# Optimization experiments

Hardware: AMD Instinct MI355X
Metric: run time of the kernel (lower is better)

## Reference

```python
import jax, jax.numpy as jnp
import numpy as np

N, G, D, H, B = 32768, 1024, 512, 768, 4   # nodes, graphs, hidden, shared, branches
GHD, NHD = 64, 3                           # graph head dim, node head dim (var_output=1)

def setup_inputs() -> dict:
    key = jax.random.key(0)
    ks = jax.random.split(key, 8)
    scale = 0.02
    x = jax.random.normal(ks[0], (N, D), dtype=jnp.float32)
    batch = jnp.sort(jax.random.randint(ks[1], (N,), 0, G, dtype=jnp.int32))
    dataset_name = jax.random.randint(ks[2], (G,), 0, B, dtype=jnp.int32)
    return {
        "x": x,
        "batch": batch,
        "dataset_name": dataset_name,
        "Wg_shared": jax.random.normal(ks[3], (B, D, H), jnp.float32) * scale,
        "bg_shared": jnp.zeros((B, H), jnp.float32),
        "Wg_head": jax.random.normal(ks[4], (B, H, 2 * GHD), jnp.float32) * scale,
        "bg_head": jnp.zeros((B, 2 * GHD), jnp.float32),
        "Wn1": jax.random.normal(ks[5], (B, D, D), jnp.float32) * scale,
        "bn1": jnp.zeros((B, D), jnp.float32),
        "Wn2": jax.random.normal(ks[6], (B, D, 2 * NHD), jnp.float32) * scale,
        "bn2": jnp.zeros((B, 2 * NHD), jnp.float32),
    }

def _select_branch(y, branch_ids):
    # y: [n, B, f], branch_ids: [n] -> [n, f]
    return jnp.take_along_axis(y, branch_ids[:, None, None], axis=1)[:, 0]

def reference(x, batch, dataset_name, Wg_shared, bg_shared, Wg_head, bg_head,
              Wn1, bn1, Wn2, bn2):
    nG = dataset_name.shape[0]
    # --- graph mean pooling (graph_pool_fn with reduction='mean') ---
    counts = jax.ops.segment_sum(jnp.ones((x.shape[0], 1), x.dtype), batch,
                                 num_segments=nG)
    x_graph = jax.ops.segment_sum(x, batch, num_segments=nG) / jnp.maximum(counts, 1.0)
    # --- graph head: per-dataset-ID branch dispatch (dense-MoE form) ---
    hg = jax.nn.relu(jnp.einsum('gd,bdh->gbh', x_graph, Wg_shared) + bg_shared)  # [G,B,H]
    hg_sel = _select_branch(hg, dataset_name)                                    # [G,H]
    og = jnp.einsum('gh,bho->gbo', hg_sel, Wg_head) + bg_head                    # [G,B,2*GHD]
    og_sel = _select_branch(og, dataset_name)
    graph_head = og_sel[:, :GHD]
    graph_var = og_sel[:, GHD:] ** 2
    # --- node head: route nodes by their graph's dataset ID (repeat_interleave) ---
    node_branch = dataset_name[batch]                                            # [N]
    hn = jax.nn.relu(jnp.einsum('nd,bdh->nbh', x, Wn1) + bn1)                    # [N,B,D]
    hn_sel = _select_branch(hn, node_branch)                                     # [N,D]
    on = jnp.einsum('nh,bho->nbo', hn_sel, Wn2) + bn2                            # [N,B,2*NHD]
    on_sel = _select_branch(on, node_branch)
    node_head = on_sel[:, :NHD]
    node_var = on_sel[:, NHD:] ** 2
    # torch returns (outputs, outputs_var); flattened here as 4 arrays
    return (graph_head, node_head, graph_var, node_var)
```

## Files before the change

kernel.cpp:

```cpp
#include <hip/hip_runtime.h>

#define N_NODES 32768
#define G_GRAPHS 1024
#define D_DIM 512
#define H_DIM 768
#define B_BR 4
#define GHD 64
#define NHD 3

#define NH_OFF (G_GRAPHS * GHD)
#define GV_OFF (G_GRAPHS * GHD + N_NODES * NHD)
#define NV_OFF (2 * G_GRAPHS * GHD + N_NODES * NHD)

typedef unsigned short ushort_t;
typedef __attribute__((ext_vector_type(8))) short short8;
typedef __attribute__((ext_vector_type(4))) float f32x4;
typedef __attribute__((ext_vector_type(4))) ushort_t ushort4_t;

__device__ __forceinline__ ushort_t rne_bf16(float v) {
  unsigned bits = __float_as_uint(v);
  return (ushort_t)((bits + 0x7fffu + ((bits >> 16) & 1u)) >> 16);
}

__global__ __launch_bounds__(1024) void segscan_kernel(
    const int* __restrict__ batch, const int* __restrict__ dsname,
    int* __restrict__ gstart, int* __restrict__ goff, int* __restrict__ glist,
    int* __restrict__ cnt, int* __restrict__ gcnt, int* __restrict__ pbase) {
  __shared__ int sg[G_GRAPHS + 1];
  __shared__ int scnt[4], sgcnt[4];
  const int tid = threadIdx.x;
  {
    int g = tid;
    int lo = 0, hi = N_NODES;
    while (lo < hi) { int mid = (lo + hi) >> 1; if (batch[mid] < g) lo = mid + 1; else hi = mid; }
    sg[g] = lo; gstart[g] = lo;
    if (tid == 0) { sg[G_GRAPHS] = N_NODES; gstart[G_GRAPHS] = N_NODES; }
  }
  __syncthreads();
  if (tid < 256) {
    const int lane = tid & 63;
    const int b = tid >> 6;
    int run_n = 0, run_g = 0;
    for (int c = 0; c < G_GRAPHS / 64; ++c) {
      int g = c * 64 + lane;
      int mine = (dsname[g] == b) ? 1 : 0;
      int len = mine ? (sg[g + 1] - sg[g]) : 0;
      int sl = len, so = mine;
#pragma unroll
      for (int off = 1; off < 64; off <<= 1) {
        int tl = __shfl_up(sl, off);
        int to = __shfl_up(so, off);
        if (lane >= off) { sl += tl; so += to; }
      }
      if (mine) {
        goff[g] = run_n + sl - len;
        glist[b * G_GRAPHS + run_g + so - 1] = g;
      }
      run_n += __shfl(sl, 63);
      run_g += __shfl(so, 63);
    }
    if (lane == 0) { scnt[b] = run_n; sgcnt[b] = run_g; }
  }
  __syncthreads();
  if (tid == 0) {
    int p = 0;
    for (int b2 = 0; b2 < 4; ++b2) {
      cnt[b2] = scnt[b2];
      gcnt[b2] = sgcnt[b2];
      pbase[b2] = p;
      p += (scnt[b2] + 63) & ~63;
    }
  }
}

__global__ __launch_bounds__(256) void prep_kernel(
    const float* __restrict__ x, const int* __restrict__ batch,
    const int* __restrict__ dsname, const int* __restrict__ gstart,
    const int* __restrict__ goff, const int* __restrict__ pbase,
    int* __restrict__ lists, ushort_t* __restrict__ xp,
    ushort_t* __restrict__ xgb,
    const float* __restrict__ Wn1, ushort_t* __restrict__ WPh,
    const float* __restrict__ Wg1, ushort_t* __restrict__ WG1,
    const float* __restrict__ Wgh, ushort_t* __restrict__ WG2,
    const float* __restrict__ Wn2, ushort_t* __restrict__ W2T) {
  __shared__ float Ws[64][65];
  const int bid = blockIdx.x;
  const int tid = threadIdx.x;

  if (bid < 1024) {
    const int rl = tid >> 6;
    const int cs = tid & 63;
    const int g = bid;
    const int start = gstart[g];
    const int len = gstart[g + 1] - start;
    const int b = dsname[g];
    const int og = goff[g];
    const int off0 = pbase[b] + og;
    float s0 = 0.f, s1 = 0.f, s2 = 0.f, s3 = 0.f;
    float s4 = 0.f, s5 = 0.f, s6 = 0.f, s7 = 0.f;
    for (int i = rl; i < len; i += 4) {
      int n = start + i;
      const float* sp = x + (size_t)n * D_DIM + cs * 8;
      float4 v0 = *reinterpret_cast<const float4*>(sp);
      float4 v1 = *reinterpret_cast<const float4*>(sp + 4);
      s0 += v0.x; s1 += v0.y; s2 += v0.z; s3 += v0.w;
      s4 += v1.x; s5 += v1.y; s6 += v1.z; s7 += v1.w;
      short8 h;
      h[0] = (short)rne_bf16(v0.x); h[1] = (short)rne_bf16(v0.y);
      h[2] = (short)rne_bf16(v0.z); h[3] = (short)rne_bf16(v0.w);
      h[4] = (short)rne_bf16(v1.x); h[5] = (short)rne_bf16(v1.y);
      h[6] = (short)rne_bf16(v1.z); h[7] = (short)rne_bf16(v1.w);
      int ib = og + i;
      *reinterpret_cast<short8*>(xp + (size_t)(off0 + i) * 512 + (cs ^ (ib & 7)) * 8) = h;
      if (cs == 0) lists[b * N_NODES + ib] = n;
    }
    float* red = (float*)Ws;
    float* rr = red + (rl * 64 + cs) * 8;
    rr[0] = s0; rr[1] = s1; rr[2] = s2; rr[3] = s3;
    rr[4] = s4; rr[5] = s5; rr[6] = s6; rr[7] = s7;
    __syncthreads();
    if (rl == 0) {
      float inv = (len > 0) ? 1.0f / (float)len : 0.0f;
      short8 h;
#pragma unroll
      for (int k = 0; k < 8; ++k) {
        float tot = red[(0 * 64 + cs) * 8 + k] + red[(1 * 64 + cs) * 8 + k] +
                    red[(2 * 64 + cs) * 8 + k] + red[(3 * 64 + cs) * 8 + k];
        h[k] = (short)rne_bf16(tot * inv);
      }
      *reinterpret_cast<short8*>(xgb + (size_t)g * D_DIM + cs * 8) = h;
    }
  } else {
    const int cid = bid - 1024;
    if (cid < 256) {
      int b = cid >> 6, t = cid & 63;
      int kt = t >> 3, nt = t & 7;
      const float* W = Wn1 + (size_t)b * D_DIM * D_DIM;
      for (int i = tid; i < 64 * 64; i += 256) {
        int k = i >> 6, n = i & 63;
        Ws[k][n] = W[(size_t)(kt * 64 + k) * D_DIM + nt * 64 + n];
      }
      __syncthreads();
      for (int i = tid; i < 64 * 8; i += 256) {
        int n = i >> 3, kq8 = i & 7;
        short8 sh;
#pragma unroll
        for (int j = 0; j < 8; ++j) sh[j] = (short)rne_bf16(Ws[kq8 * 8 + j][n]);
        int gn = nt * 64 + n, gk0 = kt * 64 + kq8 * 8;
        int n16 = gn >> 4, l15 = gn & 15;
        int ks = gk0 >> 5, lq = (gk0 >> 3) & 3;
        size_t off = ((((size_t)b * 32 + n16) * 16 + ks) * 64 + lq * 16 + l15) * 8;
        *reinterpret_cast<short8*>(WPh + off) = sh;
      }
    } else if (cid < 640) {
      int l2 = cid - 256;
      int b = l2 / 96, t = l2 % 96;
      int kt = t / 12, nt = t % 12;
      const float* W = Wg1 + (size_t)b * D_DIM * H_DIM;
      for (int i = tid; i < 64 * 64; i += 256) {
        int k = i >> 6, n = i & 63;
        Ws[k][n] = W[(size_t)(kt * 64 + k) * H_DIM + nt * 64 + n];
      }
      __syncthreads();
      for (int i = tid; i < 64 * 8; i += 256) {
        int n = i >> 3, kq8 = i & 7;
        short8 sh;
#pragma unroll
        for (int j = 0; j < 8; ++j) sh[j] = (short)rne_bf16(Ws[kq8 * 8 + j][n]);
        int gn = nt * 64 + n, gk0 = kt * 64 + kq8 * 8;
        int n16 = gn >> 4, l15 = gn & 15;
        int ks = gk0 >> 5, lq = (gk0 >> 3) & 3;
        size_t off = ((((size_t)b * 48 + n16) * 16 + ks) * 64 + lq * 16 + l15) * 8;
        *reinterpret_cast<short8*>(WG1 + off) = sh;
      }
    } else if (cid < 644) {
      int b = cid - 640;
      const float* W = Wgh + (size_t)b * H_DIM * 2 * GHD;
      for (int i = tid; i < 8 * 24 * 64; i += 256) {
        int n16 = i / (24 * 64);
        int rem = i % (24 * 64);
        int ks = rem / 64, lane = rem % 64;
        int l15 = lane & 15, lq = lane >> 4;
        int o = n16 * 16 + l15;
        short8 sv;
#pragma unroll
        for (int j = 0; j < 8; ++j) {
          int k = ks * 32 + lq * 8 + j;
          sv[j] = (short)rne_bf16(W[(size_t)k * 128 + o]);
        }
        *reinterpret_cast<short8*>(WG2 + (size_t)i * 8 + (size_t)b * (8 * 24 * 64 * 8)) = sv;
      }
    } else {
      int b = cid - 644;
      for (int i = tid; i < 16 * D_DIM; i += 256) {
        int o = i & 15, c = i >> 4;
        float v = (o < 6) ? Wn2[(size_t)b * D_DIM * 6 + c * 6 + o] : 0.0f;
        W2T[(size_t)b * 16 * D_DIM + o * D_DIM + c] = rne_bf16(v);
      }
    }
  }
}

#define NBM 64
#define GRAPH_BLOCKS 128
#define NODE_BLOCKS 576

__global__ __launch_bounds__(512, 2) void mega_kernel(
    const ushort_t* __restrict__ xpacked,
    const ushort_t* __restrict__ WPh,
    const float* __restrict__ bn1,
    const ushort_t* __restrict__ W2T, const float* __restrict__ bn2,
    const int* __restrict__ cnt, const int* __restrict__ pbase,
    const int* __restrict__ lists,
    const ushort_t* __restrict__ xgb,
    const ushort_t* __restrict__ WG1, const float* __restrict__ bg_shared,
    const ushort_t* __restrict__ WG2, const float* __restrict__ bg_head,
    const int* __restrict__ gcnt, const int* __restrict__ glist,
    float* __restrict__ out) {
  __shared__ __align__(16) char smem[131072];
  __shared__ int idxbuf[64];

  const int bid = blockIdx.x;
  const int tid = threadIdx.x;
  const int lane = tid & 63;
  const int w = tid >> 6;
  const int l15 = lane & 15;
  const int lq = lane >> 4;

  if (bid >= GRAPH_BLOCKS) {
    const int nb = bid - GRAPH_BLOCKS;
    const int b = (nb & 7) >> 1;
    const int tile = ((nb >> 3) << 1) | (nb & 1);
    const int count = cnt[b];
    const int base = tile * NBM;
    if (base >= count) return;
    const int tile_base = pbase[b] + base;

    ushort_t* Ah = (ushort_t*)smem;
    if (tid < NBM) {
      int r = base + tid;
      idxbuf[tid] = (r < count) ? lists[b * N_NODES + r] : lists[b * N_NODES];
    }

    const char* srow = (const char*)(xpacked + (size_t)tile_base * 512);
#pragma unroll
    for (int i = 0; i < 8; ++i) {
      int row = w * 8 + i;
      const void* gsrc = srow + (size_t)row * 1024 + (size_t)lane * 16;
      __builtin_amdgcn_global_load_lds(
          (const __attribute__((address_space(1))) void*)gsrc,
          (__attribute__((address_space(3))) void*)((char*)Ah + row * 1024),
          16, 0, 0);
    }
    __syncthreads();

    const ushort_t* __restrict__ wph =
        WPh + (((size_t)b * 32 + w * 4) * 16) * 512 + (size_t)lane * 8;
    ushort_t* Bl = (ushort_t*)(smem + 65536 + w * 8192);

#pragma unroll
    for (int ct = 0; ct < 4; ++ct) {
      __builtin_amdgcn_global_load_lds(
          (const __attribute__((address_space(1))) void*)(wph + (size_t)(ct * 16) * 512),
          (__attribute__((address_space(3))) void*)(Bl + ct * 512),
          16, 0, 0);
    }

    f32x4 acc[4][4];
#pragma unroll
    for (int i = 0; i < 4; ++i)
#pragma unroll
      for (int j = 0; j < 4; ++j) acc[i][j] = (f32x4){0.f, 0.f, 0.f, 0.f};

#pragma unroll
    for (int ks = 0; ks < 16; ++ks) {
      const int nks = (ks + 1) & 15;
      ushort_t* Bnx = Bl + ((ks + 1) & 1) * 2048;
#pragma unroll
      for (int ct = 0; ct < 4; ++ct) {
        __builtin_amdgcn_global_load_lds(
            (const __attribute__((address_space(1))) void*)(wph + (size_t)(ct * 16 + nks) * 512),
            (__attribute__((address_space(3))) void*)(Bnx + ct * 512),
            16, 0, 0);
      }
      asm volatile("s_waitcnt vmcnt(4)" ::: "memory");
      __builtin_amdgcn_sched_barrier(0);
      const ushort_t* Bc = Bl + (ks & 1) * 2048;
      short8 ah[4], bh[4];
#pragma unroll
      for (int rt = 0; rt < 4; ++rt) {
        int R = rt * 16 + l15;
        int byteoff = R * 1024 + ((ks * 64 + lq * 16) ^ ((R & 7) << 4));
        ah[rt] = *reinterpret_cast<const short8*>((const char*)Ah + byteoff);
      }
#pragma unroll
      for (int ct = 0; ct < 4; ++ct)
        bh[ct] = *reinterpret_cast<const short8*>(Bc + ct * 512 + lane * 8);
#pragma unroll
      for (int ct = 0; ct < 4; ++ct) {
#pragma unroll
        for (int rt = 0; rt < 4; ++rt) {
          acc[rt][ct] = __builtin_amdgcn_mfma_f32_16x16x32_bf16(ah[rt], bh[ct], acc[rt][ct], 0, 0, 0);
        }
      }
    }

    __syncthreads();
    ushort_t* hn = Ah;
#pragma unroll
    for (int ct = 0; ct < 4; ++ct) {
      int n = w * 64 + ct * 16 + l15;
      float bias = bn1[b * D_DIM + n];
#pragma unroll
      for (int rt = 0; rt < 4; ++rt) {
#pragma unroll
        for (int j = 0; j < 4; ++j) {
          int row = rt * 16 + lq * 4 + j;
          float v = fmaxf(acc[rt][ct][j] + bias, 0.0f);
          int byteoff = row * 1024 + ((n * 2) ^ ((row & 7) << 4));
          *reinterpret_cast<ushort_t*>((char*)hn + byteoff) = rne_bf16(v);
        }
      }
    }
    __syncthreads();

    if (w < 4) {
      f32x4 acc2 = (f32x4){0.f, 0.f, 0.f, 0.f};
      const ushort_t* __restrict__ w2 =
          W2T + (size_t)b * (16 * 512) + (size_t)l15 * 512 + lq * 8;
      const int R = w * 16 + l15;
#pragma unroll
      for (int ks = 0; ks < 16; ++ks) {
        int byteoff = R * 1024 + ((ks * 64 + lq * 16) ^ ((R & 7) << 4));
        short8 a2 = *reinterpret_cast<const short8*>((const char*)hn + byteoff);
        short8 b2 = *reinterpret_cast<const short8*>(w2 + ks * 32);
        acc2 = __builtin_amdgcn_mfma_f32_16x16x32_bf16(a2, b2, acc2, 0, 0, 0);
      }
      int o = l15;
      if (o < 6) {
        float bo = bn2[b * 6 + o];
#pragma unroll
        for (int j = 0; j < 4; ++j) {
          int r = w * 16 + lq * 4 + j;
          if (base + r < count) {
            int n = idxbuf[r];
            float v = acc2[j] + bo;
            if (o < NHD) out[NH_OFF + n * NHD + o] = v;
            else out[NV_OFF + n * NHD + (o - NHD)] = v * v;
          }
        }
      }
    }
  } else {
    const int gb = bid;
    const int b = (gb & 7) >> 1;
    const int tile = ((gb >> 3) << 1) | (gb & 1);
    const int gc = gcnt[b];
    const int base = tile * 32;
    if (base >= gc) return;

    ushort_t* Ag = (ushort_t*)smem;
    if (tid < 32) {
      int r = base + tid;
      idxbuf[tid] = (r < gc) ? glist[b * G_GRAPHS + r] : glist[b * G_GRAPHS];
    }
    __syncthreads();

#pragma unroll
    for (int it = 0; it < 4; ++it) {
      int u = it * 512 + tid;
      int r = u >> 6, cp = u & 63;
      const ushort_t* sp = xgb + (size_t)idxbuf[r] * D_DIM + cp * 8;
      short8 h = *reinterpret_cast<const short8*>(sp);
      int byteoff = r * 1024 + ((cp * 16) ^ ((r & 7) << 4));
      *reinterpret_cast<short8*>((char*)Ag + byteoff) = h;
    }
    __syncthreads();

    f32x4 acc[2][6];
#pragma unroll
    for (int i = 0; i < 2; ++i)
#pragma unroll
      for (int j = 0; j < 6; ++j) acc[i][j] = (f32x4){0.f, 0.f, 0.f, 0.f};

    const ushort_t* __restrict__ g1 =
        WG1 + (((size_t)b * 48 + w * 6) * 16) * 512 + (size_t)lane * 8;

    for (int ks = 0; ks < 16; ++ks) {
      short8 ah[2];
#pragma unroll
      for (int rt = 0; rt < 2; ++rt) {
        int R = rt * 16 + l15;
        int byteoff = R * 1024 + ((ks * 64 + lq * 16) ^ ((R & 7) << 4));
        ah[rt] = *reinterpret_cast<const short8*>((const char*)Ag + byteoff);
      }
#pragma unroll
      for (int ct = 0; ct < 6; ++ct) {
        short8 bh = *reinterpret_cast<const short8*>(g1 + (size_t)(ct * 16 + ks) * 512);
#pragma unroll
        for (int rt = 0; rt < 2; ++rt) {
          acc[rt][ct] = __builtin_amdgcn_mfma_f32_16x16x32_bf16(ah[rt], bh, acc[rt][ct], 0, 0, 0);
        }
      }
    }

    __syncthreads();
    ushort_t* hgs = (ushort_t*)smem;
#pragma unroll
    for (int ct = 0; ct < 6; ++ct) {
      int n = w * 96 + ct * 16 + l15;
      float bias = bg_shared[b * H_DIM + n];
#pragma unroll
      for (int rt = 0; rt < 2; ++rt) {
#pragma unroll
        for (int j = 0; j < 4; ++j) {
          int row = rt * 16 + lq * 4 + j;
          float v = fmaxf(acc[rt][ct][j] + bias, 0.0f);
          int byteoff = row * 1536 + ((n * 2) ^ ((row & 7) << 4));
          *reinterpret_cast<ushort_t*>((char*)hgs + byteoff) = rne_bf16(v);
        }
      }
    }
    __syncthreads();

    f32x4 acc2[2];
    acc2[0] = (f32x4){0.f, 0.f, 0.f, 0.f};
    acc2[1] = (f32x4){0.f, 0.f, 0.f, 0.f};
    const ushort_t* __restrict__ g2 =
        WG2 + ((size_t)(b * 8 + w) * 24 * 64 + lane) * 8;

    for (int ks = 0; ks < 24; ++ks) {
      short8 b2 = *reinterpret_cast<const short8*>(g2 + (size_t)ks * 512);
#pragma unroll
      for (int rt = 0; rt < 2; ++rt) {
        int R = rt * 16 + l15;
        int byteoff = R * 1536 + ((ks * 64 + lq * 16) ^ ((R & 7) << 4));
        short8 a2 = *reinterpret_cast<const short8*>((const char*)hgs + byteoff);
        acc2[rt] = __builtin_amdgcn_mfma_f32_16x16x32_bf16(a2, b2, acc2[rt], 0, 0, 0);
      }
    }

    int o = w * 16 + l15;
    float bo = bg_head[b * 2 * GHD + o];
#pragma unroll
    for (int rt = 0; rt < 2; ++rt) {
#pragma unroll
      for (int j = 0; j < 4; ++j) {
        int r = rt * 16 + lq * 4 + j;
        if (base + r < gc) {
          int g = idxbuf[r];
          float v = acc2[rt][j] + bo;
          if (o < GHD) out[g * GHD + o] = v;
          else out[GV_OFF + g * GHD + (o - GHD)] = v * v;
        }
      }
    }
  }
}

extern "C" void kernel_launch(void* const* d_in, const int* in_sizes, int n_in,
                              void* d_out, int out_size, void* d_ws, size_t ws_size,
                              hipStream_t stream) {
  const float* x         = (const float*)d_in[0];
  const int*   batch     = (const int*)d_in[1];
  const int*   dsname    = (const int*)d_in[2];
  const float* Wg_shared = (const float*)d_in[3];
  const float* bg_shared = (const float*)d_in[4];
  const float* Wg_head   = (const float*)d_in[5];
  const float* bg_head   = (const float*)d_in[6];
  const float* Wn1       = (const float*)d_in[7];
  const float* bn1       = (const float*)d_in[8];
  const float* Wn2       = (const float*)d_in[9];
  const float* bn2       = (const float*)d_in[10];
  float* out = (float*)d_out;

  int* ws_i   = (int*)d_ws;
  int* cnt    = ws_i;
  int* gcnt   = ws_i + 8;
  int* pbase  = ws_i + 12;
  int* gstart = ws_i + 16;
  int* goff   = ws_i + 1056;
  int* glist  = ws_i + 2080;
  int* lists  = ws_i + 6176;
  ushort_t* xgb  = (ushort_t*)(ws_i + 137248);
  ushort_t* WPh  = xgb + 524288;
  ushort_t* W2T  = WPh + 1048576;
  ushort_t* WG1  = W2T + 32768;
  ushort_t* WG2  = WG1 + 1572864;
  ushort_t* xpacked = WG2 + 393216;

  segscan_kernel<<<1, 1024, 0, stream>>>(batch, dsname, gstart, goff, glist,
                                         cnt, gcnt, pbase);
  prep_kernel<<<1672, 256, 0, stream>>>(x, batch, dsname, gstart, goff, pbase,
                                        lists, xpacked, xgb,
                                        Wn1, WPh, Wg_shared, WG1,
                                        Wg_head, WG2, Wn2, W2T);
  mega_kernel<<<GRAPH_BLOCKS + NODE_BLOCKS, 512, 0, stream>>>(
      xpacked, WPh, bn1, W2T, bn2, cnt, pbase, lists,
      xgb, WG1, bg_shared, WG2, bg_head, gcnt, glist, out);
}
```

Baseline: 91.98 us.

## Gather and convert x to bf16 inside node GEMM instead of prepacking

The prep kernel no longer writes a branch-packed bf16 copy of x. Instead, each node tile in the main kernel gathers its rows from fp32 x through the index list, converts them to bf16, and stores them into swizzled LDS. This removes a 32 MB bf16 write and its later read, at the cost of uncoalesced-by-row fp32 gathers (twice the bytes per row) and synchronous loads rather than async global-to-LDS copies inside the GEMM kernel.

```diff
diff --git a/kernel.cpp b/kernel.cpp
--- a/kernel.cpp
+++ b/kernel.cpp
@@ -76,8 +76,8 @@
 __global__ __launch_bounds__(256) void prep_kernel(
     const float* __restrict__ x, const int* __restrict__ batch,
     const int* __restrict__ dsname, const int* __restrict__ gstart,
-    const int* __restrict__ goff, const int* __restrict__ pbase,
-    int* __restrict__ lists, ushort_t* __restrict__ xp,
+    const int* __restrict__ goff,
+    int* __restrict__ lists,
     ushort_t* __restrict__ xgb,
     const float* __restrict__ Wn1, ushort_t* __restrict__ WPh,
     const float* __restrict__ Wg1, ushort_t* __restrict__ WG1,
@@ -95,24 +95,15 @@
     const int len = gstart[g + 1] - start;
     const int b = dsname[g];
     const int og = goff[g];
-    const int off0 = pbase[b] + og;
+    for (int i = tid; i < len; i += 256) lists[b * N_NODES + og + i] = start + i;
     float s0 = 0.f, s1 = 0.f, s2 = 0.f, s3 = 0.f;
     float s4 = 0.f, s5 = 0.f, s6 = 0.f, s7 = 0.f;
     for (int i = rl; i < len; i += 4) {
-      int n = start + i;
-      const float* sp = x + (size_t)n * D_DIM + cs * 8;
+      const float* sp = x + (size_t)(start + i) * D_DIM + cs * 8;
       float4 v0 = *reinterpret_cast<const float4*>(sp);
       float4 v1 = *reinterpret_cast<const float4*>(sp + 4);
       s0 += v0.x; s1 += v0.y; s2 += v0.z; s3 += v0.w;
       s4 += v1.x; s5 += v1.y; s6 += v1.z; s7 += v1.w;
-      short8 h;
-      h[0] = (short)rne_bf16(v0.x); h[1] = (short)rne_bf16(v0.y);
-      h[2] = (short)rne_bf16(v0.z); h[3] = (short)rne_bf16(v0.w);
-      h[4] = (short)rne_bf16(v1.x); h[5] = (short)rne_bf16(v1.y);
-      h[6] = (short)rne_bf16(v1.z); h[7] = (short)rne_bf16(v1.w);
-      int ib = og + i;
-      *reinterpret_cast<short8*>(xp + (size_t)(off0 + i) * 512 + (cs ^ (ib & 7)) * 8) = h;
-      if (cs == 0) lists[b * N_NODES + ib] = n;
     }
     float* red = (float*)Ws;
     float* rr = red + (rl * 64 + cs) * 8;
@@ -206,7 +197,7 @@
 #define NODE_BLOCKS 576
 
 __global__ __launch_bounds__(512, 2) void mega_kernel(
-    const ushort_t* __restrict__ xpacked,
+    const float* __restrict__ x,
     const ushort_t* __restrict__ WPh,
     const float* __restrict__ bn1,
     const ushort_t* __restrict__ W2T, const float* __restrict__ bn2,
@@ -234,23 +225,27 @@
     const int count = cnt[b];
     const int base = tile * NBM;
     if (base >= count) return;
-    const int tile_base = pbase[b] + base;
 
     ushort_t* Ah = (ushort_t*)smem;
     if (tid < NBM) {
       int r = base + tid;
       idxbuf[tid] = (r < count) ? lists[b * N_NODES + r] : lists[b * N_NODES];
     }
-
-    const char* srow = (const char*)(xpacked + (size_t)tile_base * 512);
-#pragma unroll
-    for (int i = 0; i < 8; ++i) {
-      int row = w * 8 + i;
-      const void* gsrc = srow + (size_t)row * 1024 + (size_t)lane * 16;
-      __builtin_amdgcn_global_load_lds(
-          (const __attribute__((address_space(1))) void*)gsrc,
-          (__attribute__((address_space(3))) void*)((char*)Ah + row * 1024),
-          16, 0, 0);
+    __syncthreads();
+
+#pragma unroll
+    for (int it = 0; it < 8; ++it) {
+      int u = it * 512 + tid;
+      int r = u >> 6, cp = u & 63;
+      const float* sp = x + (size_t)idxbuf[r] * D_DIM + cp * 8;
+      float4 v0 = *reinterpret_cast<const float4*>(sp);
+      float4 v1 = *reinterpret_cast<const float4*>(sp + 4);
+      short8 h;
+      h[0] = (short)rne_bf16(v0.x); h[1] = (short)rne_bf16(v0.y);
+      h[2] = (short)rne_bf16(v0.z); h[3] = (short)rne_bf16(v0.w);
+      h[4] = (short)rne_bf16(v1.x); h[5] = (short)rne_bf16(v1.y);
+      h[6] = (short)rne_bf16(v1.z); h[7] = (short)rne_bf16(v1.w);
+      *reinterpret_cast<short8*>((char*)Ah + r * 1024 + ((cp ^ (r & 7)) << 4)) = h;
     }
     __syncthreads();
 
@@ -487,15 +482,14 @@
   ushort_t* W2T  = WPh + 1048576;
   ushort_t* WG1  = W2T + 32768;
   ushort_t* WG2  = WG1 + 1572864;
-  ushort_t* xpacked = WG2 + 393216;
 
   segscan_kernel<<<1, 1024, 0, stream>>>(batch, dsname, gstart, goff, glist,
                                          cnt, gcnt, pbase);
-  prep_kernel<<<1672, 256, 0, stream>>>(x, batch, dsname, gstart, goff, pbase,
-                                        lists, xpacked, xgb,
+  prep_kernel<<<1672, 256, 0, stream>>>(x, batch, dsname, gstart, goff,
+                                        lists, xgb,
                                         Wn1, WPh, Wg_shared, WG1,
                                         Wg_head, WG2, Wn2, W2T);
   mega_kernel<<<GRAPH_BLOCKS + NODE_BLOCKS, 512, 0, stream>>>(
-      xpacked, WPh, bn1, W2T, bn2, cnt, pbase, lists,
+      x, WPh, bn1, W2T, bn2, cnt, pbase, lists,
       xgb, WG1, bg_shared, WG2, bg_head, gcnt, glist, out);
 }
```

Measured after the change: 89.40 us. -2.8%, faster.
